# Performance work log

Measured on AMD Instinct MI355X. Metric: run time of the kernel, lower is better.

The kernel has to match this reference:

```python
import jax, jax.numpy as jnp
import numpy as np

B, T, F, U = 32, 2048, 512, 512


def hard_sigmoid(x):
    # Keras hard_sigmoid: clip(0.2*x + 0.5, 0, 1)
    return jnp.clip(0.2 * x + 0.5, 0.0, 1.0)


def setup_inputs() -> dict:
    key = jax.random.key(0)
    ks = jax.random.split(key, 10)
    s = 0.05  # keep pre-activations in a sane range
    return {
        "x": jax.random.normal(ks[0], (B, F), jnp.float32),
        "h": jax.random.normal(ks[1], (B, U), jnp.float32),
        "annotations": jax.random.normal(ks[2], (B, T, F), jnp.float32),
        "kernel": jax.random.normal(ks[3], (F, 3 * U), jnp.float32) * s,
        "recurrent_kernel": jax.random.normal(ks[4], (U, 3 * U), jnp.float32) * s,
        "attention_kernel": jax.random.normal(ks[5], (F, 3 * U), jnp.float32) * s,
        "Wa": jax.random.normal(ks[6], (U, U), jnp.float32) * s,
        "Ua": jax.random.normal(ks[7], (F, U), jnp.float32) * s,
        "Va": jax.random.normal(ks[8], (U,), jnp.float32) * s,
        "bias": jnp.zeros((3 * U,), jnp.float32),
        "attention_bias": jnp.zeros((3 * U,), jnp.float32),
        "Wa_bias": jnp.zeros((U,), jnp.float32),
        "Ua_bias": jnp.zeros((U,), jnp.float32),
    }


def reference(x, h, annotations, kernel, recurrent_kernel, attention_kernel,
              Wa, Ua, Va, bias, attention_bias, Wa_bias, Ua_bias):
    u = h.shape[-1]
    # --- Bahdanau additive attention ---
    # pre: [B, T, U] = Wa h_{t-1} (broadcast over T) + Ua a_j
    pre = (h @ Wa + Wa_bias)[:, None, :] + annotations @ Ua + Ua_bias
    scores = jnp.einsum('btu,u->bt', jnp.tanh(pre), Va)          # [B, T]
    alpha = jax.nn.softmax(scores, axis=-1)                      # [B, T]
    c = jnp.einsum('bt,btf->bf', alpha, annotations)             # context [B, F]

    # --- GRU gates (reset_after=False, implementation 1 math, batched) ---
    xm = x @ kernel + bias                                       # [B, 3U]
    am = c @ attention_kernel + attention_bias                   # [B, 3U]
    x_z, x_r, x_h = xm[:, :u], xm[:, u:2 * u], xm[:, 2 * u:]
    a_z, a_r, a_h = am[:, :u], am[:, u:2 * u], am[:, 2 * u:]
    h_z = h @ recurrent_kernel[:, :u]
    h_r = h @ recurrent_kernel[:, u:2 * u]

    z = hard_sigmoid(x_z + h_z + a_z)                            # update gate
    r = hard_sigmoid(x_r + h_r + a_r)                            # reset gate
    hh = jnp.tanh(x_h + (r * h) @ recurrent_kernel[:, 2 * u:] + a_h)
    h_new = z * h + (1.0 - z) * hh
    return h_new
```

## Files before the change

### kernel.cpp

```cpp
#include <hip/hip_runtime.h>
#include <hip/hip_bf16.h>
#include <math.h>

#define BB 32
#define TT 2048
#define FF 512
#define UU 512

typedef __attribute__((ext_vector_type(4))) float f32x4;
typedef __attribute__((ext_vector_type(4))) short bf16x4;
typedef __attribute__((ext_vector_type(8))) short bf16x8;

__device__ inline short f2bf(float f) {
  union { __hip_bfloat16 h; short s; } u;
  u.h = __float2bfloat16(f);
  return u.s;
}

__device__ inline float bf2f(unsigned short s) {
  return __uint_as_float(((unsigned)s) << 16);
}

__device__ inline float tanh_fast(float x) {
  float e = __expf(2.0f * x);
  return 1.0f - 2.0f * __builtin_amdgcn_rcpf(e + 1.0f);
}


__global__ __launch_bounds__(256) void k1_hw(
    const float* __restrict__ h, const float* __restrict__ Wa,
    const float* __restrict__ Wa_bias, const float* __restrict__ Ua_bias,
    float* __restrict__ hw) {
  int idx = blockIdx.x * blockDim.x + threadIdx.x;
  int b = idx >> 9;
  int u = idx & 511;
  float acc = Wa_bias[u] + Ua_bias[u];
  const float* hrow = h + b * UU;
  for (int f = 0; f < FF; ++f) acc += hrow[f] * Wa[f * UU + u];
  hw[idx] = acc;
}

__global__ __launch_bounds__(64) void k0_pack(
    const float* __restrict__ Ua, short* __restrict__ Up) {
  const int n16 = blockIdx.x;
  const int k32 = blockIdx.y;
  const int l = threadIdx.x;
  const int n = n16 * 16 + (l & 15);
  const int g = l >> 4;
  bf16x8 v;
#pragma unroll
  for (int i = 0; i < 8; ++i) {
    int k = k32 * 32 + (i < 4 ? g * 4 + i : 16 + g * 4 + (i - 4));
    v[i] = f2bf(Ua[k * UU + n]);
  }
  *reinterpret_cast<bf16x8*>(Up + ((size_t)(n16 * 16 + k32) * 64 + l) * 8) = v;
}

__global__ __launch_bounds__(512, 2) void k2_flash(
    const float* __restrict__ ann, const short* __restrict__ Up,
    const float* __restrict__ Va, const float* __restrict__ hw,
    float* __restrict__ mbuf, float* __restrict__ lbuf,
    float* __restrict__ cpart) {
  __shared__ short Af[65536];
  __shared__ float red[8][128];
  __shared__ float e_all[128];
  __shared__ float sred[128];
  __shared__ float wtmp[4];
  __shared__ float ctxp[8][512];
  const int tile = blockIdx.x;
  const int b = blockIdx.y;
  const int t0 = tile * 128;
  const int tid = threadIdx.x;
  const int w = tid >> 6;
  const int l = tid & 63;
  const int lo = l & 15;
  const int g = l >> 4;

  const float* annb = ann + ((size_t)b * TT + t0) * FF;
  const float* srow = annb + (size_t)(w * 16 + lo) * FF + g * 4;
  short* const afw = &Af[((w * 16) * 64 + l) * 8];

  const short* upb[4];
  upb[0] = Up + ((size_t)((w * 4 + 0) * 16) * 64 + l) * 8;
  upb[1] = Up + ((size_t)((w * 4 + 1) * 16) * 64 + l) * 8;
  upb[2] = Up + ((size_t)((w * 4 + 2) * 16) * 64 + l) * 8;
  upb[3] = Up + ((size_t)((w * 4 + 3) * 16) * 64 + l) * 8;

  f32x4 acc[8][4];
#pragma unroll
  for (int mf = 0; mf < 8; ++mf)
#pragma unroll
    for (int nf = 0; nf < 4; ++nf) acc[mf][nf] = (f32x4)0.f;

  f32x4 stg[2][2];
  bf16x8 bb[2][4];

  stg[0][0] = *reinterpret_cast<const f32x4*>(srow + 0 * 32);
  stg[0][1] = *reinterpret_cast<const f32x4*>(srow + 0 * 32 + 16);
  stg[1][0] = *reinterpret_cast<const f32x4*>(srow + 1 * 32);
  stg[1][1] = *reinterpret_cast<const f32x4*>(srow + 1 * 32 + 16);
#pragma unroll
  for (int nf = 0; nf < 4; ++nf) {
    bb[0][nf] = *reinterpret_cast<const bf16x8*>(upb[nf]);
    bb[1][nf] = *reinterpret_cast<const bf16x8*>(upb[nf] + 512);
  }
  {
    bf16x8 o;
    o[0] = f2bf(stg[0][0].x); o[1] = f2bf(stg[0][0].y);
    o[2] = f2bf(stg[0][0].z); o[3] = f2bf(stg[0][0].w);
    o[4] = f2bf(stg[0][1].x); o[5] = f2bf(stg[0][1].y);
    o[6] = f2bf(stg[0][1].z); o[7] = f2bf(stg[0][1].w);
    *reinterpret_cast<bf16x8*>(afw + 0 * 512) = o;
  }
  __syncthreads();

#pragma unroll
  for (int s = 0; s < 16; ++s) {
    if (s < 14) {
      stg[s & 1][0] = *reinterpret_cast<const f32x4*>(srow + (s + 2) * 32);
      stg[s & 1][1] = *reinterpret_cast<const f32x4*>(srow + (s + 2) * 32 + 16);
    }
    bf16x8 aA[8];
#pragma unroll
    for (int mf = 0; mf < 8; ++mf)
      aA[mf] = *reinterpret_cast<const bf16x8*>(
          &Af[((mf * 16 + s) * 64 + l) * 8]);
    __builtin_amdgcn_s_setprio(1);
#pragma unroll
    for (int mf = 0; mf < 8; ++mf)
#pragma unroll
      for (int nf = 0; nf < 4; ++nf)
        acc[mf][nf] = __builtin_amdgcn_mfma_f32_16x16x32_bf16(
            aA[mf], bb[s & 1][nf], acc[mf][nf], 0, 0, 0);
    __builtin_amdgcn_s_setprio(0);
    if (s < 14) {
#pragma unroll
      for (int nf = 0; nf < 4; ++nf)
        bb[s & 1][nf] =
            *reinterpret_cast<const bf16x8*>(upb[nf] + (s + 2) * 512);
    }
    if (s < 15) {
      const f32x4 c0 = stg[(s + 1) & 1][0];
      const f32x4 c1 = stg[(s + 1) & 1][1];
      bf16x8 o;
      o[0] = f2bf(c0.x); o[1] = f2bf(c0.y); o[2] = f2bf(c0.z); o[3] = f2bf(c0.w);
      o[4] = f2bf(c1.x); o[5] = f2bf(c1.y); o[6] = f2bf(c1.z); o[7] = f2bf(c1.w);
      *reinterpret_cast<bf16x8*>(afw + (s + 1) * 512) = o;
      asm volatile("s_waitcnt lgkmcnt(0)" ::: "memory");
      __builtin_amdgcn_s_barrier();
    }
  }
  __syncthreads();

  const float* hwb = hw + b * UU;
  float part[8][4];
#pragma unroll
  for (int mf = 0; mf < 8; ++mf)
#pragma unroll
    for (int r = 0; r < 4; ++r) part[mf][r] = 0.f;
#pragma unroll
  for (int nf = 0; nf < 4; ++nf) {
    const int u = w * 64 + nf * 16 + lo;
    const float hv = hwb[u];
    const float vv = Va[u];
#pragma unroll
    for (int mf = 0; mf < 8; ++mf)
#pragma unroll
      for (int r = 0; r < 4; ++r)
        part[mf][r] += tanh_fast(acc[mf][nf][r] + hv) * vv;
  }
#pragma unroll
  for (int mf = 0; mf < 8; ++mf)
#pragma unroll
    for (int r = 0; r < 4; ++r) {
      float s = part[mf][r];
      s += __shfl_xor(s, 1);
      s += __shfl_xor(s, 2);
      s += __shfl_xor(s, 4);
      s += __shfl_xor(s, 8);
      part[mf][r] = s;
    }
  if (lo == 0) {
#pragma unroll
    for (int mf = 0; mf < 8; ++mf)
#pragma unroll
      for (int r = 0; r < 4; ++r)
        red[w][mf * 16 + g * 4 + r] = part[mf][r];
  }
  __syncthreads();

  if (tid < 128) {
    float s = red[0][tid] + red[1][tid] + red[2][tid] + red[3][tid] +
              red[4][tid] + red[5][tid] + red[6][tid] + red[7][tid];
    sred[tid] = s;
    float m = s;
#pragma unroll
    for (int off = 1; off < 64; off <<= 1) m = fmaxf(m, __shfl_xor(m, off));
    if ((tid & 63) == 0) wtmp[tid >> 6] = m;
  }
  __syncthreads();
  if (tid < 128) {
    float m = fmaxf(wtmp[0], wtmp[1]);
    float e = __expf(sred[tid] - m);
    e_all[tid] = e;
    float ls = e;
#pragma unroll
    for (int off = 1; off < 64; off <<= 1) ls += __shfl_xor(ls, off);
    if ((tid & 63) == 0) wtmp[2 + (tid >> 6)] = ls;
    if (tid == 0) mbuf[b * 16 + tile] = m;
  }
  __syncthreads();
  if (tid == 0) lbuf[b * 16 + tile] = wtmp[2] + wtmp[3];

  {
    const int fo = tid & 63;
    const int ts = tid >> 6;
    const int kk2 = fo >> 2;
    const int gg = fo & 3;
    float a8[8];
#pragma unroll
    for (int j = 0; j < 8; ++j) a8[j] = 0.f;
#pragma unroll
    for (int it = 0; it < 16; ++it) {
      const int tl = (it + fo) & 15;
      const int t = ts * 16 + tl;
      const int entry = (ts * 16 + kk2) * 64 + gg * 16 + tl;
      bf16x8 v = *reinterpret_cast<const bf16x8*>(&Af[entry * 8]);
      const float e = e_all[t];
#pragma unroll
      for (int j = 0; j < 8; ++j)
        a8[j] += e * bf2f((unsigned short)v[j]);
    }
#pragma unroll
    for (int j = 0; j < 8; ++j) ctxp[ts][fo * 8 + j] = a8[j];
  }
  __syncthreads();
  {
    float s = 0.f;
#pragma unroll
    for (int ts2 = 0; ts2 < 8; ++ts2) s += ctxp[ts2][tid];
    const int fo2 = tid >> 3;
    const int j2 = tid & 7;
    const int f = (fo2 >> 2) * 32 +
                  ((j2 < 4) ? (fo2 & 3) * 4 + j2 : 16 + (fo2 & 3) * 4 + (j2 - 4));
    cpart[(size_t)(b * 16 + tile) * 512 + f] = s;
  }
}

__global__ __launch_bounds__(256) void k6_combine(
    const float* __restrict__ mbuf, const float* __restrict__ lbuf,
    const float* __restrict__ cpart, float* __restrict__ c) {
  const int b = blockIdx.x;
  const int tid = threadIdx.x;
  __shared__ float sm[16], sl[16];
  if (tid < 16) {
    sm[tid] = mbuf[b * 16 + tid];
    sl[tid] = lbuf[b * 16 + tid];
  }
  __syncthreads();
  float M = -1e30f;
#pragma unroll
  for (int i = 0; i < 16; ++i) M = fmaxf(M, sm[i]);
  float D = 0.f;
#pragma unroll
  for (int i = 0; i < 16; ++i) D += __expf(sm[i] - M) * sl[i];
  const float inv = 1.f / D;
  const int f = tid * 2;
  float a0 = 0.f, a1 = 0.f;
#pragma unroll
  for (int i = 0; i < 16; ++i) {
    const float wi = __expf(sm[i] - M);
    const float2 v = *reinterpret_cast<const float2*>(
        &cpart[(size_t)(b * 16 + i) * 512 + f]);
    a0 += wi * v.x;
    a1 += wi * v.y;
  }
  c[b * FF + f]     = a0 * inv;
  c[b * FF + f + 1] = a1 * inv;
}

__global__ __launch_bounds__(512) void k5a_gates(
    const float* __restrict__ x, const float* __restrict__ cc,
    const float* __restrict__ h, const float* __restrict__ kern,
    const float* __restrict__ ak, const float* __restrict__ rk,
    float* __restrict__ Gp) {
  __shared__ float wsx[64][64], wsa[64][64], wsr[64][64];
  __shared__ float xs[32][64], cs[32][64], hs[32][64];
  const int n0 = blockIdx.x * 64;
  const int kg = blockIdx.y;
  const int kg0 = kg * 64;
  const bool has_r = (n0 < 1024);
  const int tid = threadIdx.x;
  const int n = tid & 63;
  const int b0 = (tid >> 6) * 4;
  const int wrow = tid >> 3, wcol = (tid & 7) * 8;
  const int orow = tid >> 4, ocol = (tid & 15) * 4;
  float acc[4] = {0.f, 0.f, 0.f, 0.f};

  {
    const size_t wb = (size_t)(kg0 + wrow) * 1536 + n0 + wcol;
    *reinterpret_cast<float4*>(&wsx[wrow][wcol])     = *reinterpret_cast<const float4*>(kern + wb);
    *reinterpret_cast<float4*>(&wsx[wrow][wcol + 4]) = *reinterpret_cast<const float4*>(kern + wb + 4);
    *reinterpret_cast<float4*>(&wsa[wrow][wcol])     = *reinterpret_cast<const float4*>(ak + wb);
    *reinterpret_cast<float4*>(&wsa[wrow][wcol + 4]) = *reinterpret_cast<const float4*>(ak + wb + 4);
    if (has_r) {
      *reinterpret_cast<float4*>(&wsr[wrow][wcol])     = *reinterpret_cast<const float4*>(rk + wb);
      *reinterpret_cast<float4*>(&wsr[wrow][wcol + 4]) = *reinterpret_cast<const float4*>(rk + wb + 4);
    }
    *reinterpret_cast<float4*>(&xs[orow][ocol]) =
        *reinterpret_cast<const float4*>(x + orow * FF + kg0 + ocol);
    *reinterpret_cast<float4*>(&cs[orow][ocol]) =
        *reinterpret_cast<const float4*>(cc + orow * FF + kg0 + ocol);
    *reinterpret_cast<float4*>(&hs[orow][ocol]) =
        *reinterpret_cast<const float4*>(h + orow * UU + kg0 + ocol);
  }
  __syncthreads();
  if (has_r) {
#pragma unroll 8
    for (int k = 0; k < 64; ++k) {
      const float wx = wsx[k][n], wa = wsa[k][n], wr = wsr[k][n];
#pragma unroll
      for (int j = 0; j < 4; ++j)
        acc[j] += xs[b0 + j][k] * wx + cs[b0 + j][k] * wa + hs[b0 + j][k] * wr;
    }
  } else {
#pragma unroll 8
    for (int k = 0; k < 64; ++k) {
      const float wx = wsx[k][n], wa = wsa[k][n];
#pragma unroll
      for (int j = 0; j < 4; ++j)
        acc[j] += xs[b0 + j][k] * wx + cs[b0 + j][k] * wa;
    }
  }
#pragma unroll
  for (int j = 0; j < 4; ++j)
    Gp[(size_t)kg * 49152 + (size_t)(b0 + j) * 1536 + n0 + n] = acc[j];
}

__global__ __launch_bounds__(256) void k5b_zr(
    const float* __restrict__ Gp, const float* __restrict__ h,
    const float* __restrict__ bias, const float* __restrict__ abias,
    float* __restrict__ zs, float* __restrict__ rh) {
  int idx = blockIdx.x * blockDim.x + threadIdx.x;
  int b = idx >> 9;
  int u = idx & 511;
  float sz = bias[u] + abias[u];
  float sr = bias[512 + u] + abias[512 + u];
  const float* gb = Gp + (size_t)b * 1536;
#pragma unroll
  for (int p = 0; p < 8; ++p) {
    sz += gb[(size_t)p * 49152 + u];
    sr += gb[(size_t)p * 49152 + 512 + u];
  }
  float z = fminf(fmaxf(0.2f * sz + 0.5f, 0.f), 1.f);
  float r = fminf(fmaxf(0.2f * sr + 0.5f, 0.f), 1.f);
  zs[idx] = z;
  rh[idx] = r * h[idx];
}

__global__ __launch_bounds__(512) void k5c_q(
    const float* __restrict__ rh, const float* __restrict__ rk,
    float* __restrict__ qp) {
  __shared__ float wsr[64][64];
  __shared__ float rs[32][64];
  const int n0 = blockIdx.x * 64;
  const int kg = blockIdx.y;
  const int kg0 = kg * 64;
  const int tid = threadIdx.x;
  const int n = tid & 63;
  const int b0 = (tid >> 6) * 4;
  const int wrow = tid >> 3, wcol = (tid & 7) * 8;
  const int orow = tid >> 4, ocol = (tid & 15) * 4;
  float acc[4] = {0.f, 0.f, 0.f, 0.f};

  {
    const size_t wb = (size_t)(kg0 + wrow) * 1536 + 1024 + n0 + wcol;
    *reinterpret_cast<float4*>(&wsr[wrow][wcol])     = *reinterpret_cast<const float4*>(rk + wb);
    *reinterpret_cast<float4*>(&wsr[wrow][wcol + 4]) = *reinterpret_cast<const float4*>(rk + wb + 4);
    *reinterpret_cast<float4*>(&rs[orow][ocol]) =
        *reinterpret_cast<const float4*>(rh + orow * UU + kg0 + ocol);
  }
  __syncthreads();
#pragma unroll 8
  for (int k = 0; k < 64; ++k) {
    const float w = wsr[k][n];
#pragma unroll
    for (int j = 0; j < 4; ++j) acc[j] += rs[b0 + j][k] * w;
  }
#pragma unroll
  for (int j = 0; j < 4; ++j)
    qp[(size_t)kg * 16384 + (b0 + j) * UU + n0 + n] = acc[j];
}

__global__ __launch_bounds__(256) void k5d_out(
    const float* __restrict__ Gp, const float* __restrict__ qp,
    const float* __restrict__ zs, const float* __restrict__ h,
    const float* __restrict__ bias, const float* __restrict__ abias,
    float* __restrict__ out) {
  int idx = blockIdx.x * blockDim.x + threadIdx.x;
  int b = idx >> 9;
  int u = idx & 511;
  float sh = bias[1024 + u] + abias[1024 + u];
  const float* gb = Gp + (size_t)b * 1536;
  const float* qb = qp + (size_t)b * 512;
#pragma unroll
  for (int p = 0; p < 8; ++p) {
    sh += gb[(size_t)p * 49152 + 1024 + u];
    sh += qb[(size_t)p * 16384 + u];
  }
  float hh = tanhf(sh);
  float z = zs[idx];
  out[idx] = z * h[idx] + (1.f - z) * hh;
}

extern "C" void kernel_launch(void* const* d_in, const int* in_sizes, int n_in,
                              void* d_out, int out_size, void* d_ws, size_t ws_size,
                              hipStream_t stream) {
  const float* x       = (const float*)d_in[0];
  const float* h       = (const float*)d_in[1];
  const float* ann     = (const float*)d_in[2];
  const float* kern    = (const float*)d_in[3];
  const float* rk      = (const float*)d_in[4];
  const float* ak      = (const float*)d_in[5];
  const float* Wa      = (const float*)d_in[6];
  const float* Ua      = (const float*)d_in[7];
  const float* Va      = (const float*)d_in[8];
  const float* bias    = (const float*)d_in[9];
  const float* abias   = (const float*)d_in[10];
  const float* Wa_bias = (const float*)d_in[11];
  const float* Ua_bias = (const float*)d_in[12];

  float* ws     = (float*)d_ws;
  float* hw     = ws;
  float* mbuf   = ws + 16384;
  float* lbuf   = ws + 16896;
  float* cpart  = ws + 17408;
  float* c      = ws + 279552;
  float* Gp     = ws + 295936;
  float* qp     = ws + 689152;
  float* zs     = ws + 820224;
  float* rh     = ws + 836608;
  short* Up     = (short*)(ws + 852992);

  dim3 g0(32, 16);
  k0_pack<<<g0, 64, 0, stream>>>(Ua, Up);

  k1_hw<<<64, 256, 0, stream>>>(h, Wa, Wa_bias, Ua_bias, hw);

  dim3 g2(TT / 128, BB);
  k2_flash<<<g2, 512, 0, stream>>>(ann, Up, Va, hw, mbuf, lbuf, cpart);

  k6_combine<<<BB, 256, 0, stream>>>(mbuf, lbuf, cpart, c);

  dim3 g5a(24, 8);
  k5a_gates<<<g5a, 512, 0, stream>>>(x, c, h, kern, ak, rk, Gp);

  k5b_zr<<<64, 256, 0, stream>>>(Gp, h, bias, abias, zs, rh);

  dim3 g5c(8, 8);
  k5c_q<<<g5c, 512, 0, stream>>>(rh, rk, qp);

  k5d_out<<<64, 256, 0, stream>>>(Gp, qp, zs, h, bias, abias, (float*)d_out);
}
```

Measured before the change: 94.48 us.

## Fuse small kernels to cut launch count from eight to five

Merges the Ua bf16 packing and the h·Wa projection into one launch split by block index. The softmax-combine step now runs inside the gates GEMM kernel, and the z/r gate computation is folded into the reset-GEMM and output kernels. The aim is to remove launch overhead and the intermediate c/zs/rh round trips through global memory for a small, latency-bound tail. In exchange, every gates block recomputes the softmax normalisation and context slice, which duplicates some cpart reads.

Result: no change. 96.29 us (+1.9%).

```diff
diff --git a/kernel.cpp b/kernel.cpp
--- a/kernel.cpp
+++ b/kernel.cpp
@@ -27,33 +27,37 @@
 }
 
 
-__global__ __launch_bounds__(256) void k1_hw(
+__global__ __launch_bounds__(256) void k01(
+    const float* __restrict__ Ua, short* __restrict__ Up,
     const float* __restrict__ h, const float* __restrict__ Wa,
     const float* __restrict__ Wa_bias, const float* __restrict__ Ua_bias,
     float* __restrict__ hw) {
-  int idx = blockIdx.x * blockDim.x + threadIdx.x;
-  int b = idx >> 9;
-  int u = idx & 511;
-  float acc = Wa_bias[u] + Ua_bias[u];
-  const float* hrow = h + b * UU;
-  for (int f = 0; f < FF; ++f) acc += hrow[f] * Wa[f * UU + u];
-  hw[idx] = acc;
-}
-
-__global__ __launch_bounds__(64) void k0_pack(
-    const float* __restrict__ Ua, short* __restrict__ Up) {
-  const int n16 = blockIdx.x;
-  const int k32 = blockIdx.y;
-  const int l = threadIdx.x;
-  const int n = n16 * 16 + (l & 15);
-  const int g = l >> 4;
-  bf16x8 v;
-#pragma unroll
-  for (int i = 0; i < 8; ++i) {
-    int k = k32 * 32 + (i < 4 ? g * 4 + i : 16 + g * 4 + (i - 4));
-    v[i] = f2bf(Ua[k * UU + n]);
-  }
-  *reinterpret_cast<bf16x8*>(Up + ((size_t)(n16 * 16 + k32) * 64 + l) * 8) = v;
+  const int bid = blockIdx.x;
+  const int tid = threadIdx.x;
+  if (bid < 128) {
+    const int cell = bid * 4 + (tid >> 6);
+    const int n16 = cell >> 4;
+    const int k32 = cell & 15;
+    const int l = tid & 63;
+    const int n = n16 * 16 + (l & 15);
+    const int g = l >> 4;
+    bf16x8 v;
+#pragma unroll
+    for (int i = 0; i < 8; ++i) {
+      int k = k32 * 32 + (i < 4 ? g * 4 + i : 16 + g * 4 + (i - 4));
+      v[i] = f2bf(Ua[k * UU + n]);
+    }
+    *reinterpret_cast<bf16x8*>(Up + ((size_t)cell * 64 + l) * 8) = v;
+  } else {
+    int idx = (bid - 128) * 256 + tid;
+    int b = idx >> 9;
+    int u = idx & 511;
+    float acc = Wa_bias[u] + Ua_bias[u];
+    const float* hrow = h + b * UU;
+#pragma unroll 8
+    for (int f = 0; f < FF; ++f) acc += hrow[f] * Wa[f * UU + u];
+    hw[idx] = acc;
+  }
 }
 
 __global__ __launch_bounds__(512, 2) void k2_flash(
@@ -247,45 +251,15 @@
   }
 }
 
-__global__ __launch_bounds__(256) void k6_combine(
-    const float* __restrict__ mbuf, const float* __restrict__ lbuf,
-    const float* __restrict__ cpart, float* __restrict__ c) {
-  const int b = blockIdx.x;
-  const int tid = threadIdx.x;
-  __shared__ float sm[16], sl[16];
-  if (tid < 16) {
-    sm[tid] = mbuf[b * 16 + tid];
-    sl[tid] = lbuf[b * 16 + tid];
-  }
-  __syncthreads();
-  float M = -1e30f;
-#pragma unroll
-  for (int i = 0; i < 16; ++i) M = fmaxf(M, sm[i]);
-  float D = 0.f;
-#pragma unroll
-  for (int i = 0; i < 16; ++i) D += __expf(sm[i] - M) * sl[i];
-  const float inv = 1.f / D;
-  const int f = tid * 2;
-  float a0 = 0.f, a1 = 0.f;
-#pragma unroll
-  for (int i = 0; i < 16; ++i) {
-    const float wi = __expf(sm[i] - M);
-    const float2 v = *reinterpret_cast<const float2*>(
-        &cpart[(size_t)(b * 16 + i) * 512 + f]);
-    a0 += wi * v.x;
-    a1 += wi * v.y;
-  }
-  c[b * FF + f]     = a0 * inv;
-  c[b * FF + f + 1] = a1 * inv;
-}
-
 __global__ __launch_bounds__(512) void k5a_gates(
-    const float* __restrict__ x, const float* __restrict__ cc,
+    const float* __restrict__ x, const float* __restrict__ mbuf,
+    const float* __restrict__ lbuf, const float* __restrict__ cpart,
     const float* __restrict__ h, const float* __restrict__ kern,
     const float* __restrict__ ak, const float* __restrict__ rk,
     float* __restrict__ Gp) {
   __shared__ float wsx[64][64], wsa[64][64], wsr[64][64];
   __shared__ float xs[32][64], cs[32][64], hs[32][64];
+  __shared__ float lsm[512], lsl[512], lwinv[512];
   const int n0 = blockIdx.x * 64;
   const int kg = blockIdx.y;
   const int kg0 = kg * 64;
@@ -297,6 +271,9 @@
   const int orow = tid >> 4, ocol = (tid & 15) * 4;
   float acc[4] = {0.f, 0.f, 0.f, 0.f};
 
+  lsm[tid] = mbuf[tid];
+  lsl[tid] = lbuf[tid];
+
   {
     const size_t wb = (size_t)(kg0 + wrow) * 1536 + n0 + wcol;
     *reinterpret_cast<float4*>(&wsx[wrow][wcol])     = *reinterpret_cast<const float4*>(kern + wb);
@@ -309,12 +286,40 @@
     }
     *reinterpret_cast<float4*>(&xs[orow][ocol]) =
         *reinterpret_cast<const float4*>(x + orow * FF + kg0 + ocol);
-    *reinterpret_cast<float4*>(&cs[orow][ocol]) =
-        *reinterpret_cast<const float4*>(cc + orow * FF + kg0 + ocol);
     *reinterpret_cast<float4*>(&hs[orow][ocol]) =
         *reinterpret_cast<const float4*>(h + orow * UU + kg0 + ocol);
   }
   __syncthreads();
+
+  if (tid < 32) {
+    float M = -1e30f;
+#pragma unroll
+    for (int i = 0; i < 16; ++i) M = fmaxf(M, lsm[tid * 16 + i]);
+    float D = 0.f;
+#pragma unroll
+    for (int i = 0; i < 16; ++i)
+      D += __expf(lsm[tid * 16 + i] - M) * lsl[tid * 16 + i];
+    const float inv = 1.f / D;
+#pragma unroll
+    for (int i = 0; i < 16; ++i)
+      lwinv[tid * 16 + i] = __expf(lsm[tid * 16 + i] - M) * inv;
+  }
+  __syncthreads();
+
+  {
+    float4 cv = {0.f, 0.f, 0.f, 0.f};
+#pragma unroll
+    for (int i = 0; i < 16; ++i) {
+      const float wi = lwinv[orow * 16 + i];
+      const float4 cp = *reinterpret_cast<const float4*>(
+          &cpart[(size_t)(orow * 16 + i) * 512 + kg0 + ocol]);
+      cv.x += wi * cp.x; cv.y += wi * cp.y;
+      cv.z += wi * cp.z; cv.w += wi * cp.w;
+    }
+    *reinterpret_cast<float4*>(&cs[orow][ocol]) = cv;
+  }
+  __syncthreads();
+
   if (has_r) {
 #pragma unroll 8
     for (int k = 0; k < 64; ++k) {
@@ -337,30 +342,10 @@
     Gp[(size_t)kg * 49152 + (size_t)(b0 + j) * 1536 + n0 + n] = acc[j];
 }
 
-__global__ __launch_bounds__(256) void k5b_zr(
+__global__ __launch_bounds__(512) void k5c_q(
     const float* __restrict__ Gp, const float* __restrict__ h,
     const float* __restrict__ bias, const float* __restrict__ abias,
-    float* __restrict__ zs, float* __restrict__ rh) {
-  int idx = blockIdx.x * blockDim.x + threadIdx.x;
-  int b = idx >> 9;
-  int u = idx & 511;
-  float sz = bias[u] + abias[u];
-  float sr = bias[512 + u] + abias[512 + u];
-  const float* gb = Gp + (size_t)b * 1536;
-#pragma unroll
-  for (int p = 0; p < 8; ++p) {
-    sz += gb[(size_t)p * 49152 + u];
-    sr += gb[(size_t)p * 49152 + 512 + u];
-  }
-  float z = fminf(fmaxf(0.2f * sz + 0.5f, 0.f), 1.f);
-  float r = fminf(fmaxf(0.2f * sr + 0.5f, 0.f), 1.f);
-  zs[idx] = z;
-  rh[idx] = r * h[idx];
-}
-
-__global__ __launch_bounds__(512) void k5c_q(
-    const float* __restrict__ rh, const float* __restrict__ rk,
-    float* __restrict__ qp) {
+    const float* __restrict__ rk, float* __restrict__ qp) {
   __shared__ float wsr[64][64];
   __shared__ float rs[32][64];
   const int n0 = blockIdx.x * 64;
@@ -377,8 +362,23 @@
     const size_t wb = (size_t)(kg0 + wrow) * 1536 + 1024 + n0 + wcol;
     *reinterpret_cast<float4*>(&wsr[wrow][wcol])     = *reinterpret_cast<const float4*>(rk + wb);
     *reinterpret_cast<float4*>(&wsr[wrow][wcol + 4]) = *reinterpret_cast<const float4*>(rk + wb + 4);
-    *reinterpret_cast<float4*>(&rs[orow][ocol]) =
-        *reinterpret_cast<const float4*>(rh + orow * UU + kg0 + ocol);
+  }
+  {
+    const int u = kg0 + ocol;
+    float4 sr = *reinterpret_cast<const float4*>(bias + 512 + u);
+    const float4 ab = *reinterpret_cast<const float4*>(abias + 512 + u);
+    sr.x += ab.x; sr.y += ab.y; sr.z += ab.z; sr.w += ab.w;
+#pragma unroll
+    for (int p = 0; p < 8; ++p) {
+      const float4 gp4 = *reinterpret_cast<const float4*>(
+          Gp + (size_t)p * 49152 + (size_t)orow * 1536 + 512 + u);
+      sr.x += gp4.x; sr.y += gp4.y; sr.z += gp4.z; sr.w += gp4.w;
+    }
+    const float4 hv = *reinterpret_cast<const float4*>(h + orow * UU + u);
+    rs[orow][ocol]     = fminf(fmaxf(0.2f * sr.x + 0.5f, 0.f), 1.f) * hv.x;
+    rs[orow][ocol + 1] = fminf(fmaxf(0.2f * sr.y + 0.5f, 0.f), 1.f) * hv.y;
+    rs[orow][ocol + 2] = fminf(fmaxf(0.2f * sr.z + 0.5f, 0.f), 1.f) * hv.z;
+    rs[orow][ocol + 3] = fminf(fmaxf(0.2f * sr.w + 0.5f, 0.f), 1.f) * hv.w;
   }
   __syncthreads();
 #pragma unroll 8
@@ -394,22 +394,22 @@
 
 __global__ __launch_bounds__(256) void k5d_out(
     const float* __restrict__ Gp, const float* __restrict__ qp,
-    const float* __restrict__ zs, const float* __restrict__ h,
-    const float* __restrict__ bias, const float* __restrict__ abias,
-    float* __restrict__ out) {
+    const float* __restrict__ h, const float* __restrict__ bias,
+    const float* __restrict__ abias, float* __restrict__ out) {
   int idx = blockIdx.x * blockDim.x + threadIdx.x;
   int b = idx >> 9;
   int u = idx & 511;
+  float sz = bias[u] + abias[u];
   float sh = bias[1024 + u] + abias[1024 + u];
   const float* gb = Gp + (size_t)b * 1536;
   const float* qb = qp + (size_t)b * 512;
 #pragma unroll
   for (int p = 0; p < 8; ++p) {
-    sh += gb[(size_t)p * 49152 + 1024 + u];
-    sh += qb[(size_t)p * 16384 + u];
-  }
+    sz += gb[(size_t)p * 49152 + u];
+    sh += gb[(size_t)p * 49152 + 1024 + u] + qb[(size_t)p * 16384 + u];
+  }
+  float z = fminf(fmaxf(0.2f * sz + 0.5f, 0.f), 1.f);
   float hh = tanhf(sh);
-  float z = zs[idx];
   out[idx] = z * h[idx] + (1.f - z) * hh;
 }
 
@@ -435,30 +435,20 @@
   float* mbuf   = ws + 16384;
   float* lbuf   = ws + 16896;
   float* cpart  = ws + 17408;
-  float* c      = ws + 279552;
-  float* Gp     = ws + 295936;
-  float* qp     = ws + 689152;
-  float* zs     = ws + 820224;
-  float* rh     = ws + 836608;
-  short* Up     = (short*)(ws + 852992);
-
-  dim3 g0(32, 16);
-  k0_pack<<<g0, 64, 0, stream>>>(Ua, Up);
-
-  k1_hw<<<64, 256, 0, stream>>>(h, Wa, Wa_bias, Ua_bias, hw);
+  float* Gp     = ws + 279552;
+  float* qp     = ws + 672768;
+  short* Up     = (short*)(ws + 803840);
+
+  k01<<<192, 256, 0, stream>>>(Ua, Up, h, Wa, Wa_bias, Ua_bias, hw);
 
   dim3 g2(TT / 128, BB);
   k2_flash<<<g2, 512, 0, stream>>>(ann, Up, Va, hw, mbuf, lbuf, cpart);
 
-  k6_combine<<<BB, 256, 0, stream>>>(mbuf, lbuf, cpart, c);
-
   dim3 g5a(24, 8);
-  k5a_gates<<<g5a, 512, 0, stream>>>(x, c, h, kern, ak, rk, Gp);
-
-  k5b_zr<<<64, 256, 0, stream>>>(Gp, h, bias, abias, zs, rh);
+  k5a_gates<<<g5a, 512, 0, stream>>>(x, mbuf, lbuf, cpart, h, kern, ak, rk, Gp);
 
   dim3 g5c(8, 8);
-  k5c_q<<<g5c, 512, 0, stream>>>(rh, rk, qp);
-
-  k5d_out<<<64, 256, 0, stream>>>(Gp, qp, zs, h, bias, abias, (float*)d_out);
-}
+  k5c_q<<<g5c, 512, 0, stream>>>(Gp, h, bias, abias, rk, qp);
+
+  k5d_out<<<64, 256, 0, stream>>>(Gp, qp, h, bias, abias, (float*)d_out);
+}
```
